# Kernel optimization log

Hardware: AMD Instinct MI355X
Metric: run time of the kernel (lower is better)

Reference implementation:

```python
import jax, jax.numpy as jnp
import numpy as np

DIM = 768
STRIDE = 1
WEIGHT_BITS = 5
FRACTION = 16   # quant_bits=16 fixed-point fraction bits for activations
INTEGER = 16
SHIFT_MIN = -(2 ** (WEIGHT_BITS - 1) - 2)  # -14
SHIFT_MAX = 0


def round_to_fixed(x, fraction=FRACTION, integer=INTEGER):
    # DeepShift-style fixed-point activation quantization
    delta = 2.0 ** (-fraction)
    bound = 2.0 ** (integer - 1)
    rounded = jnp.floor(x / delta + 0.5) * delta
    return jnp.clip(rounded, -bound, bound - 1)


def round_power_of_2(w):
    # quantize weight to sign * 2^shift, shift clamped to 5-bit shift range
    sign = jnp.sign(w)
    shift = jnp.clip(jnp.round(jnp.log2(jnp.abs(w) + 1e-32)), SHIFT_MIN, SHIFT_MAX)
    return sign * (2.0 ** shift)


def ste(x, xq):
    # straight-through estimator: forward uses xq, backward passes grads to x
    return x + jax.lax.stop_gradient(xq - x)


def setup_inputs() -> dict:
    key = jax.random.key(0)
    k1, k2, k3 = jax.random.split(key, 3)
    x = jax.random.normal(k1, (32, DIM, 56, 56), dtype=jnp.float32)
    # kaiming-ish fan-in init for depthwise 3x3 (fan_in = 9)
    weight = jax.random.normal(k2, (DIM, 1, 3, 3), dtype=jnp.float32) * (1.0 / 3.0)
    bias = jax.random.normal(k3, (DIM,), dtype=jnp.float32) * 0.02
    return {"x": x, "weight": weight, "bias": bias}


def reference(x, weight, bias):
    xq = ste(x, round_to_fixed(x))
    wq = ste(weight, round_power_of_2(weight))
    out = jax.lax.conv_general_dilated(
        xq, wq,
        window_strides=(STRIDE, STRIDE),
        padding=((1, 1), (1, 1)),
        feature_group_count=DIM,
        dimension_numbers=("NCHW", "OIHW", "NCHW"),
    )
    return out + bias[None, :, None, None]
```

## Files before the change

kernel.cpp:

```cpp
#include <hip/hip_runtime.h>
#include <math.h>

#define DIM 768
#define HWS 56
#define PLANE (HWS * HWS)
#define PLANE4 (PLANE / 4)
#define LSTRIDE 64
#define LROWS 59

__device__ __forceinline__ float quant_fixed(float x) {
    float t = x * 65536.0f;
    t = t + 0.5f;
    t = floorf(t);
    float r = t * (1.0f / 65536.0f);
    r = fmaxf(r, -32768.0f);
    r = fminf(r, 32767.0f);
    return r;
}

__global__ __launch_bounds__(256, 8) void peg_shift_dwconv(
        const float* __restrict__ x, const float* __restrict__ weight,
        const float* __restrict__ bias, float* __restrict__ out) {
    __shared__ __align__(16) float tile[LROWS * LSTRIDE];
    __shared__ float qw_s[9];
    __shared__ float bias_s;

    const int tid = threadIdx.x;
    const int plane = blockIdx.x;
    const int c = plane % DIM;

    if (tid < 192) {
        int r = tid >> 6;
        int row = (r == 2) ? 58 : r;
        tile[row * LSTRIDE + (tid & 63)] = 0.0f;
    }
    for (int i = tid; i < 448; i += 256) {
        int row = 2 + (i >> 3);
        int col = 56 + (i & 7);
        tile[row * LSTRIDE + col] = 0.0f;
    }
    if (tid < 9) {
        float wv = weight[c * 9 + tid];
        float a = fabsf(wv) + 1e-32f;
        float sh = rintf(log2f(a));
        sh = fminf(fmaxf(sh, -14.0f), 0.0f);
        float p = exp2f(sh);
        float s = (wv > 0.0f) ? 1.0f : ((wv < 0.0f) ? -1.0f : 0.0f);
        qw_s[tid] = s * p;
    }
    if (tid == 9) bias_s = bias[c];

    const float4* in4 = (const float4*)(x + (size_t)plane * PLANE);
    for (int j = tid; j < PLANE4; j += 256) {
        float4 v = in4[j];
        v.x = quant_fixed(v.x);
        v.y = quant_fixed(v.y);
        v.z = quant_fixed(v.z);
        v.w = quant_fixed(v.w);
        int h = j / 14;
        int q = j - h * 14;
        *(float4*)&tile[(h + 2) * LSTRIDE + q * 4] = v;
    }
    __syncthreads();

    float k[9];
    #pragma unroll
    for (int i = 0; i < 9; ++i) k[i] = qw_s[i];
    const float bv = bias_s;

    const int w = tid & 63;
    const int strip = tid >> 6;
    const bool is_active = (w < HWS);
    const int wc = is_active ? w : 0;
    const int h0 = strip * 14;
    float* outp = out + (size_t)plane * PLANE;

    int ra = (h0 + 1) * LSTRIDE + wc;
    int rb = (h0 + 2) * LSTRIDE + wc;
    float a0 = tile[ra - 1], a1 = tile[ra], a2 = tile[ra + 1];
    float b0 = tile[rb - 1], b1 = tile[rb], b2 = tile[rb + 1];

    #pragma unroll
    for (int h = h0; h < h0 + 14; ++h) {
        int rc = (h + 3) * LSTRIDE + wc;
        float c0 = tile[rc - 1], c1 = tile[rc], c2 = tile[rc + 1];
        float acc = bv;
        acc += k[0] * a0; acc += k[1] * a1; acc += k[2] * a2;
        acc += k[3] * b0; acc += k[4] * b1; acc += k[5] * b2;
        acc += k[6] * c0; acc += k[7] * c1; acc += k[8] * c2;
        if (is_active) outp[h * HWS + w] = acc;
        a0 = b0; a1 = b1; a2 = b2;
        b0 = c0; b1 = c1; b2 = c2;
    }
}

extern "C" void kernel_launch(void* const* d_in, const int* in_sizes, int n_in,
                              void* d_out, int out_size, void* d_ws, size_t ws_size,
                              hipStream_t stream) {
    const float* x = (const float*)d_in[0];
    const float* wgt = (const float*)d_in[1];
    const float* bias = (const float*)d_in[2];
    float* out = (float*)d_out;
    const int nplanes = in_sizes[0] / PLANE;
    peg_shift_dwconv<<<nplanes, 256, 0, stream>>>(x, wgt, bias, out);
}
```

Before: 491.7 us.

## Use single-wavefront blocks with register-batched loads and float4 output strips

Shrinks each plane's block from 256 to 64 threads. Each thread issues 12 float4 global loads up front, which gives more memory-level parallelism per thread. In the compute phase, 56 threads each produce four adjacent outputs per row with float4 LDS reads and float4 stores, reusing loaded neighbours across outputs. The trade-off is much higher register use per thread and fewer threads per plane, so latency hiding depends on how many blocks fit on each CU, which the LDS tile size limits.

```diff
diff --git a/kernel.cpp b/kernel.cpp
--- a/kernel.cpp
+++ b/kernel.cpp
@@ -9,16 +9,12 @@
 #define LROWS 59
 
 __device__ __forceinline__ float quant_fixed(float x) {
-    float t = x * 65536.0f;
-    t = t + 0.5f;
-    t = floorf(t);
+    float t = floorf(x * 65536.0f + 0.5f);
     float r = t * (1.0f / 65536.0f);
-    r = fmaxf(r, -32768.0f);
-    r = fminf(r, 32767.0f);
-    return r;
+    return fminf(fmaxf(r, -32768.0f), 32767.0f);
 }
 
-__global__ __launch_bounds__(256, 8) void peg_shift_dwconv(
+__global__ __launch_bounds__(64, 2) void peg_shift_dwconv(
         const float* __restrict__ x, const float* __restrict__ weight,
         const float* __restrict__ bias, float* __restrict__ out) {
     __shared__ __align__(16) float tile[LROWS * LSTRIDE];
@@ -29,16 +25,13 @@
     const int plane = blockIdx.x;
     const int c = plane % DIM;
 
-    if (tid < 192) {
-        int r = tid >> 6;
-        int row = (r == 2) ? 58 : r;
-        tile[row * LSTRIDE + (tid & 63)] = 0.0f;
+    for (int f = tid; f < 160; f += 64) {
+        int row, col4;
+        if (f < 48) { int r = f >> 4; row = (r == 2) ? 58 : r; col4 = f & 15; }
+        else        { int g = f - 48; row = 2 + (g >> 1);      col4 = 14 + (g & 1); }
+        *(float4*)&tile[row * LSTRIDE + col4 * 4] = float4{0.f, 0.f, 0.f, 0.f};
     }
-    for (int i = tid; i < 448; i += 256) {
-        int row = 2 + (i >> 3);
-        int col = 56 + (i & 7);
-        tile[row * LSTRIDE + col] = 0.0f;
-    }
+
     if (tid < 9) {
         float wv = weight[c * 9 + tid];
         float a = fabsf(wv) + 1e-32f;
@@ -51,46 +44,78 @@
     if (tid == 9) bias_s = bias[c];
 
     const float4* in4 = (const float4*)(x + (size_t)plane * PLANE);
-    for (int j = tid; j < PLANE4; j += 256) {
-        float4 v = in4[j];
-        v.x = quant_fixed(v.x);
-        v.y = quant_fixed(v.y);
-        v.z = quant_fixed(v.z);
-        v.w = quant_fixed(v.w);
-        int h = j / 14;
-        int q = j - h * 14;
-        *(float4*)&tile[(h + 2) * LSTRIDE + q * 4] = v;
+    float4 v[12];
+    #pragma unroll
+    for (int k = 0; k < 12; ++k) v[k] = in4[k * 64 + tid];
+    float4 vt;
+    if (tid < 16) vt = in4[768 + tid];
+
+    #pragma unroll
+    for (int k = 0; k < 12; ++k) {
+        int j = k * 64 + tid;
+        int h = j / 14, q = j - h * 14;
+        float4 w4;
+        w4.x = quant_fixed(v[k].x); w4.y = quant_fixed(v[k].y);
+        w4.z = quant_fixed(v[k].z); w4.w = quant_fixed(v[k].w);
+        *(float4*)&tile[(h + 2) * LSTRIDE + q * 4] = w4;
+    }
+    if (tid < 16) {
+        int j = 768 + tid;
+        int h = j / 14, q = j - h * 14;
+        float4 w4;
+        w4.x = quant_fixed(vt.x); w4.y = quant_fixed(vt.y);
+        w4.z = quant_fixed(vt.z); w4.w = quant_fixed(vt.w);
+        *(float4*)&tile[(h + 2) * LSTRIDE + q * 4] = w4;
     }
     __syncthreads();
 
-    float k[9];
+    float kk[9];
     #pragma unroll
-    for (int i = 0; i < 9; ++i) k[i] = qw_s[i];
+    for (int i = 0; i < 9; ++i) kk[i] = qw_s[i];
     const float bv = bias_s;
 
-    const int w = tid & 63;
-    const int strip = tid >> 6;
-    const bool is_active = (w < HWS);
-    const int wc = is_active ? w : 0;
-    const int h0 = strip * 14;
-    float* outp = out + (size_t)plane * PLANE;
+    if (tid < 56) {
+        const int s    = tid % 14;
+        const int band = tid / 14;
+        const int c0   = 4 * s;
+        float* outp = out + (size_t)plane * PLANE;
 
-    int ra = (h0 + 1) * LSTRIDE + wc;
-    int rb = (h0 + 2) * LSTRIDE + wc;
-    float a0 = tile[ra - 1], a1 = tile[ra], a2 = tile[ra + 1];
-    float b0 = tile[rb - 1], b1 = tile[rb], b2 = tile[rb + 1];
+        const float* rowp = tile + (band * 14 + 1) * LSTRIDE + c0;
+        float  l0 = rowp[-1];
+        float4 m0 = *(const float4*)rowp;
+        float  r0 = rowp[4];
+        rowp += LSTRIDE;
+        float  l1 = rowp[-1];
+        float4 m1 = *(const float4*)rowp;
+        float  r1 = rowp[4];
 
-    #pragma unroll
-    for (int h = h0; h < h0 + 14; ++h) {
-        int rc = (h + 3) * LSTRIDE + wc;
-        float c0 = tile[rc - 1], c1 = tile[rc], c2 = tile[rc + 1];
-        float acc = bv;
-        acc += k[0] * a0; acc += k[1] * a1; acc += k[2] * a2;
-        acc += k[3] * b0; acc += k[4] * b1; acc += k[5] * b2;
-        acc += k[6] * c0; acc += k[7] * c1; acc += k[8] * c2;
-        if (is_active) outp[h * HWS + w] = acc;
-        a0 = b0; a1 = b1; a2 = b2;
-        b0 = c0; b1 = c1; b2 = c2;
+        #pragma unroll
+        for (int i = 0; i < 14; ++i) {
+            rowp += LSTRIDE;
+            float  l2 = rowp[-1];
+            float4 m2 = *(const float4*)rowp;
+            float  r2 = rowp[4];
+            const int h = band * 14 + i;
+
+            float4 acc;
+            acc.x = bv + kk[0]*l0   + kk[1]*m0.x + kk[2]*m0.y
+                       + kk[3]*l1   + kk[4]*m1.x + kk[5]*m1.y
+                       + kk[6]*l2   + kk[7]*m2.x + kk[8]*m2.y;
+            acc.y = bv + kk[0]*m0.x + kk[1]*m0.y + kk[2]*m0.z
+                       + kk[3]*m1.x + kk[4]*m1.y + kk[5]*m1.z
+                       + kk[6]*m2.x + kk[7]*m2.y + kk[8]*m2.z;
+            acc.z = bv + kk[0]*m0.y + kk[1]*m0.z + kk[2]*m0.w
+                       + kk[3]*m1.y + kk[4]*m1.z + kk[5]*m1.w
+                       + kk[6]*m2.y + kk[7]*m2.z + kk[8]*m2.w;
+            acc.w = bv + kk[0]*m0.z + kk[1]*m0.w + kk[2]*r0
+                       + kk[3]*m1.z + kk[4]*m1.w + kk[5]*r1
+                       + kk[6]*m2.z + kk[7]*m2.w + kk[8]*r2;
+
+            *(float4*)&outp[h * HWS + c0] = acc;
+
+            l0 = l1; m0 = m1; r0 = r1;
+            l1 = l2; m1 = m2; r1 = r2;
+        }
     }
 }
 
@@ -102,5 +127,5 @@
     const float* bias = (const float*)d_in[2];
     float* out = (float*)d_out;
     const int nplanes = in_sizes[0] / PLANE;
-    peg_shift_dwconv<<<nplanes, 256, 0, stream>>>(x, wgt, bias, out);
+    peg_shift_dwconv<<<nplanes, 64, 0, stream>>>(x, wgt, bias, out);
 }
```

New measurement: 494.0 us. Within noise of the previous version (+0.5%).
